# Optimization experiments

Hardware: AMD Instinct MI355X
Metric: run time of the kernel (lower is better)

## Reference

```python
import jax, jax.numpy as jnp
import numpy as np

NW, K, C, H = 4096, 32, 256, 8
HD = C // H
POS_BND = 25            # int(0.8 * patch_size * dilation**0.5) = int(0.8*32)
RPE_NUM = 2 * POS_BND + 1  # 51; table has 3*51 = 153 rows


def setup_inputs() -> dict:
    key = jax.random.key(0)
    ks = jax.random.split(key, 10)
    s = 0.02
    return {
        "data": jax.random.normal(ks[0], (NW * K, C), jnp.float32),
        "mask": jax.random.normal(ks[1], (NW, K, K), jnp.float32),
        "rel_pos": jax.random.randint(ks[2], (NW, K, K, 3), -POS_BND, POS_BND + 1, jnp.int32),
        "qkv_w": jax.random.normal(ks[3], (C, 3 * C), jnp.float32) * s,
        "qkv_b": jnp.zeros((3 * C,), jnp.float32),
        "proj_w": jax.random.normal(ks[4], (C, C), jnp.float32) * s,
        "proj_b": jnp.zeros((C,), jnp.float32),
        "rpe_table": jax.random.normal(ks[5], (3 * RPE_NUM, H), jnp.float32) * s,
        "ln1_g": jnp.ones((C,), jnp.float32),
        "ln1_b": jnp.zeros((C,), jnp.float32),
        "ln2_g": jnp.ones((C,), jnp.float32),
        "ln2_b": jnp.zeros((C,), jnp.float32),
        "fc1_w": jax.random.normal(ks[6], (C, 4 * C), jnp.float32) * s,
        "fc1_b": jnp.zeros((4 * C,), jnp.float32),
        "fc2_w": jax.random.normal(ks[7], (4 * C, C), jnp.float32) * s,
        "fc2_b": jnp.zeros((C,), jnp.float32),
    }


def _ln(x, g, b):
    m = jnp.mean(x, axis=-1, keepdims=True)
    v = jnp.var(x, axis=-1, keepdims=True)
    return (x - m) * jax.lax.rsqrt(v + 1e-5) * g + b


def reference(data, mask, rel_pos, qkv_w, qkv_b, proj_w, proj_b, rpe_table,
              ln1_g, ln1_b, ln2_g, ln2_b, fc1_w, fc1_b, fc2_w, fc2_b):
    scale = float(HD) ** -0.5
    # pre-norm attention branch
    x = _ln(data, ln1_g, ln1_b)
    qkv = (x @ qkv_w + qkv_b).reshape(NW, K, 3, H, HD)
    q, k, v = qkv[:, :, 0], qkv[:, :, 1], qkv[:, :, 2]   # [NW,K,H,HD]
    attn = jnp.einsum('wqhd,wkhd->whqk', q * scale, k)   # [NW,H,K,K]
    # RPE: clamp xyz offsets, offset each axis into its table band, gather+sum
    idx = jnp.clip(rel_pos, -POS_BND, POS_BND) + POS_BND + jnp.arange(3) * RPE_NUM
    bias = rpe_table[idx].sum(axis=3)                    # [NW,K,K,H]
    attn = attn + bias.transpose(0, 3, 1, 2) + mask[:, None]
    attn = jax.nn.softmax(attn, axis=-1)
    out = jnp.einsum('whqk,wkhd->wqhd', attn, v).reshape(NW * K, C)
    data = data + (out @ proj_w + proj_b)
    # pre-norm MLP branch
    h = _ln(data, ln2_g, ln2_b)
    h = jax.nn.gelu(h @ fc1_w + fc1_b) @ fc2_w + fc2_b
    return data + h
```

## Files before the change

kernel.cpp:

```cpp
#include <hip/hip_runtime.h>

#define NWIN 4096
#define KTOK 32
#define CH 256
#define NH 8
#define NTOK (NWIN*KTOK)

typedef unsigned short bf16u;
typedef __attribute__((ext_vector_type(4))) float f32x4;
typedef __attribute__((ext_vector_type(4))) unsigned short u16x4;
typedef __attribute__((ext_vector_type(8))) unsigned short u16x8;
typedef __attribute__((ext_vector_type(8))) __bf16 bf16x8;

__device__ __forceinline__ unsigned short f2bf(float f) {
  unsigned u = __builtin_bit_cast(unsigned, f);
  u += 0x7fffu + ((u >> 16) & 1u);
  return (unsigned short)(u >> 16);
}

__device__ __forceinline__ f32x4 mfma16(bf16x8 a, bf16x8 b, f32x4 c) {
  return __builtin_amdgcn_mfma_f32_16x16x32_bf16(a, b, c, 0, 0, 0);
}

__device__ __forceinline__ void gl16(const void* g, void* l) {
  __builtin_amdgcn_global_load_lds(
      (const __attribute__((address_space(1))) unsigned int*)g,
      (__attribute__((address_space(3))) unsigned int*)l, 16, 0, 0);
}

__device__ __forceinline__ float gelu_f(float x) {
  float u = x + 0.044715f * x * x * x;
  return x * __builtin_amdgcn_rcpf(1.f + __expf(-1.5957691216057308f * u));
}

__global__ __launch_bounds__(256) void wprep_kernel(const float* __restrict__ W,
                                                    bf16u* __restrict__ Wt,
                                                    int Kd, int Nd) {
  int idx = blockIdx.x * 256 + threadIdx.x;
  if (idx >= Kd * Nd) return;
  int k = idx / Nd, n = idx - k * Nd;
  Wt[n * Kd + k] = f2bf(W[idx]);
}

__global__ __launch_bounds__(256) void ln_kernel(const float* __restrict__ x,
                                                 const float* __restrict__ g,
                                                 const float* __restrict__ b,
                                                 bf16u* __restrict__ y) {
  const int row = blockIdx.x * 4 + (threadIdx.x >> 6);
  const int lane = threadIdx.x & 63;
  const size_t base = (size_t)row * CH + lane * 4;
  const f32x4 v = *(const f32x4*)(x + base);
  float s = v[0] + v[1] + v[2] + v[3];
  float q = v[0]*v[0] + v[1]*v[1] + v[2]*v[2] + v[3]*v[3];
  #pragma unroll
  for (int d = 32; d; d >>= 1) { s += __shfl_xor(s, d); q += __shfl_xor(q, d); }
  const float mean = s * (1.f/256.f);
  const float rs = rsqrtf(q * (1.f/256.f) - mean*mean + 1e-5f);
  const f32x4 gv = *(const f32x4*)(g + lane*4);
  const f32x4 bv = *(const f32x4*)(b + lane*4);
  u16x4 o;
  #pragma unroll
  for (int d = 0; d < 4; ++d) o[d] = f2bf((v[d]-mean)*rs*gv[d] + bv[d]);
  *(u16x4*)(y + base) = o;
}

template<int EPI>
__global__ __launch_bounds__(256, 3)
void gemm_kernel(const bf16u* __restrict__ A, const bf16u* __restrict__ Bt,
                 const float* __restrict__ bias, const float* __restrict__ resid,
                 void* __restrict__ out, int M, int N, int K, int nx) {
  __shared__ __align__(16) char lds[49152];
  const int tid = threadIdx.x;
  const int lane = tid & 63;
  const int wv = tid >> 6;
  const int lo = lane & 15, hi = lane >> 4;
  const int nwg = gridDim.x;
  const int cpx = nwg >> 3;
  const int swz = (blockIdx.x & 7) * cpx + (blockIdx.x >> 3);
  const int by = swz / nx, bx = swz - by * nx;
  const int bm = by * 128, bn = bx * 128;
  const int wm = (wv >> 1) * 64, wn = (wv & 1) * 64;

  f32x4 acc[4][4] = {};

  const int srow = tid >> 2;
  const int sk = (tid & 3) * 16;
  const size_t rstep = (size_t)64 * K * 2;
  const char* gA = (const char*)(A + (size_t)(bm + srow) * K) + sk;
  const char* gB = (const char*)(Bt + (size_t)(bn + srow) * K) + sk;

  auto STAGE = [&](int b, int kt) {
    char* As = lds + b * 16384;
    char* Bs = As + 8192;
    const char* ga = gA + kt * 64;
    const char* gb = gB + kt * 64;
    gl16(ga,         As + tid*16);
    gl16(ga + rstep, As + 4096 + tid*16);
    gl16(gb,         Bs + tid*16);
    gl16(gb + rstep, Bs + 4096 + tid*16);
  };

  const int nt = K >> 5;
  STAGE(0, 0);
  STAGE(1, 1);
  int cur = 0;
  for (int t = 0; t < nt; ++t) {
    if (t + 2 < nt) {
      STAGE((cur + 2) % 3, t + 2);
      asm volatile("s_waitcnt vmcnt(8)" ::: "memory");
    } else if (t + 1 < nt) {
      asm volatile("s_waitcnt vmcnt(4)" ::: "memory");
    } else {
      asm volatile("s_waitcnt vmcnt(0)" ::: "memory");
    }
    __builtin_amdgcn_sched_barrier(0);
    __builtin_amdgcn_s_barrier();
    const char* As = lds + cur * 16384;
    const char* Bs = As + 8192;
    bf16x8 af[4], bfv[4];
    #pragma unroll
    for (int i = 0; i < 4; ++i) {
      af[i]  = *(const bf16x8*)(As + (wm + i*16 + lo)*64 + hi*16);
      bfv[i] = *(const bf16x8*)(Bs + (wn + i*16 + lo)*64 + hi*16);
    }
    #pragma unroll
    for (int i = 0; i < 4; ++i)
      #pragma unroll
      for (int j = 0; j < 4; ++j)
        acc[i][j] = mfma16(af[i], bfv[j], acc[i][j]);
    __builtin_amdgcn_s_barrier();
    cur = (cur + 1) % 3;
  }

  __syncthreads();
  float* Ls = (float*)(lds + wv * 4352);
  const int mb = bm + wm, nb = bn + wn;
  const int lrow = lane >> 3;
  const int lcol = (lane & 7) * 8;
  const f32x4 bv0 = *(const f32x4*)(bias + nb + lcol);
  const f32x4 bv1 = *(const f32x4*)(bias + nb + lcol + 4);

  #pragma unroll
  for (int i = 0; i < 4; ++i) {
    #pragma unroll
    for (int j = 0; j < 4; ++j)
      #pragma unroll
      for (int r = 0; r < 4; ++r)
        Ls[(hi*4 + r)*68 + j*16 + lo] = acc[i][j][r];
    #pragma unroll
    for (int p = 0; p < 2; ++p) {
      const int rr = p*8 + lrow;
      const int m = mb + i*16 + rr;
      f32x4 v0 = *(const f32x4*)(Ls + rr*68 + lcol);
      f32x4 v1 = *(const f32x4*)(Ls + rr*68 + lcol + 4);
      v0 += bv0; v1 += bv1;
      if constexpr (EPI == 2) {
        const float* rp = resid + (size_t)m*N + nb + lcol;
        v0 += *(const f32x4*)rp;
        v1 += *(const f32x4*)(rp + 4);
        float* op = (float*)out + (size_t)m*N + nb + lcol;
        *(f32x4*)op = v0;
        *(f32x4*)(op + 4) = v1;
      } else {
        if constexpr (EPI == 1) {
          #pragma unroll
          for (int d = 0; d < 4; ++d) { v0[d] = gelu_f(v0[d]); v1[d] = gelu_f(v1[d]); }
        }
        u16x8 o8;
        #pragma unroll
        for (int d = 0; d < 4; ++d) { o8[d] = f2bf(v0[d]); o8[4+d] = f2bf(v1[d]); }
        *(u16x8*)((bf16u*)out + (size_t)m*N + nb + lcol) = o8;
      }
    }
  }
}

__global__ __launch_bounds__(256, 2)
void gemmP_kernel(const bf16u* __restrict__ A, const bf16u* __restrict__ Bt,
                  const float* __restrict__ bias, const float* __restrict__ resid,
                  float* __restrict__ out, bf16u* __restrict__ xln,
                  const float* __restrict__ g2, const float* __restrict__ b2) {
  __shared__ __align__(16) char lds[73728];
  const int tid = threadIdx.x, lane = tid & 63, wv = tid >> 6;
  const int lo = lane & 15, hi = lane >> 4;
  const int nwg = gridDim.x, cpx = nwg >> 3;
  const int by = (blockIdx.x & 7) * cpx + (blockIdx.x >> 3);
  const int bm = by * 128;
  const int wmh = wv >> 1;
  const int wm = wmh * 64, wn = (wv & 1) * 128;

  f32x4 acc[4][8] = {};

  const int arow = tid >> 2;
  const int sk = (tid & 3) * 16;
  const char* gA = (const char*)(A + (size_t)(bm + arow) * 256) + sk;
  const char* gB = (const char*)(Bt + (size_t)arow * 256) + sk;

  auto STAGE = [&](int b, int kt) {
    char* As = lds + b * 24576;
    char* Bs = As + 8192;
    const char* ga = gA + kt * 64;
    const char* gb = gB + kt * 64;
    gl16(ga,         As + arow*64 + sk);
    gl16(ga + 32768, As + 4096 + arow*64 + sk);
    #pragma unroll
    for (int p = 0; p < 4; ++p)
      gl16(gb + p*32768, Bs + p*4096 + arow*64 + sk);
  };

  STAGE(0, 0);
  STAGE(1, 1);
  int cur = 0;
  for (int t = 0; t < 8; ++t) {
    if (t + 2 < 8) {
      STAGE((cur + 2) % 3, t + 2);
      asm volatile("s_waitcnt vmcnt(12)" ::: "memory");
    } else if (t + 1 < 8) {
      asm volatile("s_waitcnt vmcnt(6)" ::: "memory");
    } else {
      asm volatile("s_waitcnt vmcnt(0)" ::: "memory");
    }
    __builtin_amdgcn_sched_barrier(0);
    __builtin_amdgcn_s_barrier();
    const char* As = lds + cur * 24576;
    const char* Bs = As + 8192;
    bf16x8 af[4], bf8[8];
    #pragma unroll
    for (int i = 0; i < 4; ++i)
      af[i] = *(const bf16x8*)(As + (wm + i*16 + lo)*64 + hi*16);
    #pragma unroll
    for (int j = 0; j < 8; ++j)
      bf8[j] = *(const bf16x8*)(Bs + (wn + j*16 + lo)*64 + hi*16);
    #pragma unroll
    for (int i = 0; i < 4; ++i)
      #pragma unroll
      for (int j = 0; j < 8; ++j)
        acc[i][j] = mfma16(af[i], bf8[j], acc[i][j]);
    __builtin_amdgcn_s_barrier();
    cur = (cur + 1) % 3;
  }

  __syncthreads();
  float* LsE = (float*)lds;
  const int c4 = (tid & 3) * 4;
  const int row64 = tid >> 2;
  const int reg = row64 >> 5, rloc = row64 & 31;
  #pragma unroll
  for (int rr = 0; rr < 2; ++rr) {
    #pragma unroll
    for (int i2 = 0; i2 < 2; ++i2) {
      const int i = rr*2 + i2;
      #pragma unroll
      for (int j = 0; j < 8; ++j)
        #pragma unroll
        for (int r = 0; r < 4; ++r)
          LsE[wmh*8320 + (i2*16 + hi*4 + r)*260 + wn + j*16 + lo] = acc[i][j][r];
    }
    __syncthreads();
    const int grow = bm + reg*64 + rr*32 + rloc;
    f32x4 d2[16];
    float sum = 0.f, sq = 0.f;
    #pragma unroll
    for (int k = 0; k < 16; ++k) {
      const int col = c4 + k*16;
      f32x4 v = *(const f32x4*)&LsE[reg*8320 + rloc*260 + col];
      v += *(const f32x4*)(bias + col);
      v += *(const f32x4*)(resid + (size_t)grow*256 + col);
      d2[k] = v;
      sum += v[0] + v[1] + v[2] + v[3];
      sq  += v[0]*v[0] + v[1]*v[1] + v[2]*v[2] + v[3]*v[3];
      *(f32x4*)(out + (size_t)grow*256 + col) = v;
    }
    sum += __shfl_xor(sum, 1); sq += __shfl_xor(sq, 1);
    sum += __shfl_xor(sum, 2); sq += __shfl_xor(sq, 2);
    const float mean = sum * (1.f/256.f);
    const float rs = rsqrtf(sq * (1.f/256.f) - mean*mean + 1e-5f);
    #pragma unroll
    for (int k = 0; k < 16; ++k) {
      const int col = c4 + k*16;
      const f32x4 gv = *(const f32x4*)(g2 + col);
      const f32x4 bv = *(const f32x4*)(b2 + col);
      u16x4 o;
      #pragma unroll
      for (int d = 0; d < 4; ++d)
        o[d] = f2bf((d2[k][d] - mean) * rs * gv[d] + bv[d]);
      *(u16x4*)(xln + (size_t)grow*256 + col) = o;
    }
    __syncthreads();
  }
}

__global__ __launch_bounds__(256, 2)
void attn_kernel(const bf16u* __restrict__ qkv, const float* __restrict__ mask,
                 const int* __restrict__ relp, const float* __restrict__ rpe,
                 bf16u* __restrict__ outp) {
  const int w = blockIdx.x;
  const int tid = threadIdx.x, lane = tid & 63, wv = tid >> 6;
  const int lo = lane & 15, hi = lane >> 4;

  __shared__ __align__(16) bf16u sQK[32*520];
  __shared__ __align__(16) bf16u sV[32][264];
  __shared__ __align__(16) bf16u sP[4][32][44];
  __shared__ float sTabT[8][156];
  __shared__ int sRel[1024];
  __shared__ float sMask[32][33];

  const size_t qbase = (size_t)w * (32*768);
  {
    #pragma unroll
    for (int t = 0; t < 8; ++t) {
      int i = tid + t*256;
      int tok = i >> 6;
      int cb = (i & 63) * 16;
      *(u16x8*)((char*)sQK + tok*1040 + cb) =
          *(const u16x8*)((const char*)(qkv + qbase) + tok*1536 + cb);
    }
    #pragma unroll
    for (int t = 0; t < 4; ++t) {
      int i = tid + t*256;
      int tok = i >> 5, c8 = i & 31;
      *(u16x8*)&sV[tok][c8*8] = *(const u16x8*)(qkv + qbase + tok*768 + 512 + c8*8);
    }
    for (int i = tid; i < 1224; i += 256)
      sTabT[i & 7][i >> 3] = rpe[i];
    #pragma unroll
    for (int t = 0; t < 4; ++t) {
      int i = tid + t*256;
      const int* rp = relp + ((size_t)w*1024 + i)*3;
      int r0 = rp[0], r1 = rp[1], r2 = rp[2];
      r0 = min(max(r0, -25), 25) + 25;
      r1 = min(max(r1, -25), 25) + 76;
      r2 = min(max(r2, -25), 25) + 127;
      sRel[i] = r0 | (r1 << 8) | (r2 << 16);
    }
    #pragma unroll
    for (int d = 0; d < 4; ++d) {
      int i = tid*4 + d;
      sMask[i >> 5][i & 31] = mask[(size_t)w*1024 + i];
    }
  }
  __syncthreads();

  const float scale = 0.17677669529663687f;
  #pragma unroll
  for (int e = 0; e < 2; ++e) {
    const int h = wv*2 + e;
    bf16x8 qf[2], kf[2];
    #pragma unroll
    for (int rf = 0; rf < 2; ++rf) {
      int tok = rf*16 + lo;
      qf[rf] = *(const bf16x8*)((const char*)sQK + tok*1040 + h*64 + hi*16);
      kf[rf] = *(const bf16x8*)((const char*)sQK + tok*1040 + 512 + h*64 + hi*16);
    }
    f32x4 S[2][2] = {};
    #pragma unroll
    for (int rf = 0; rf < 2; ++rf)
      #pragma unroll
      for (int cf = 0; cf < 2; ++cf)
        S[rf][cf] = mfma16(qf[rf], kf[cf], S[rf][cf]);
    #pragma unroll
    for (int rf = 0; rf < 2; ++rf)
      #pragma unroll
      for (int cf = 0; cf < 2; ++cf)
        #pragma unroll
        for (int r = 0; r < 4; ++r) {
          const int qq = rf*16 + hi*4 + r;
          const int kk = cf*16 + lo;
          const int pk = sRel[qq*32 + kk];
          const float bsum = sTabT[h][pk & 255] + sTabT[h][(pk >> 8) & 255]
                           + sTabT[h][(pk >> 16) & 255];
          S[rf][cf][r] = S[rf][cf][r] * scale + bsum + sMask[qq][kk];
        }
    #pragma unroll
    for (int rf = 0; rf < 2; ++rf)
      #pragma unroll
      for (int r = 0; r < 4; ++r) {
        float m0 = fmaxf(S[rf][0][r], S[rf][1][r]);
        #pragma unroll
        for (int d = 1; d < 16; d <<= 1) m0 = fmaxf(m0, __shfl_xor(m0, d));
        const float p0 = __expf(S[rf][0][r] - m0);
        const float p1 = __expf(S[rf][1][r] - m0);
        float ss = p0 + p1;
        #pragma unroll
        for (int d = 1; d < 16; d <<= 1) ss += __shfl_xor(ss, d);
        const float inv = 1.f / ss;
        S[rf][0][r] = p0 * inv;
        S[rf][1][r] = p1 * inv;
      }
    #pragma unroll
    for (int rf = 0; rf < 2; ++rf)
      #pragma unroll
      for (int cf = 0; cf < 2; ++cf)
        #pragma unroll
        for (int r = 0; r < 4; ++r)
          sP[wv][rf*16 + hi*4 + r][cf*16 + lo] = f2bf(S[rf][cf][r]);
    f32x4 O[2][2] = {};
    #pragma unroll
    for (int rf = 0; rf < 2; ++rf) {
      bf16x8 pf;
      *(u16x4*)&pf       = *(const u16x4*)&sP[wv][rf*16 + lo][hi*8];
      *((u16x4*)&pf + 1) = *(const u16x4*)&sP[wv][rf*16 + lo][hi*8 + 4];
      #pragma unroll
      for (int cf = 0; cf < 2; ++cf) {
        bf16x8 vf;
        #pragma unroll
        for (int j = 0; j < 8; ++j)
          ((bf16u*)&vf)[j] = sV[hi*8 + j][h*32 + cf*16 + lo];
        O[rf][cf] = mfma16(pf, vf, O[rf][cf]);
      }
    }
    #pragma unroll
    for (int rf = 0; rf < 2; ++rf)
      #pragma unroll
      for (int cf = 0; cf < 2; ++cf)
        #pragma unroll
        for (int r = 0; r < 4; ++r) {
          const int qq = rf*16 + hi*4 + r;
          outp[(size_t)(w*32 + qq)*256 + h*32 + cf*16 + lo] = f2bf(O[rf][cf][r]);
        }
  }
}

extern "C" void kernel_launch(void* const* d_in, const int* in_sizes, int n_in,
                              void* d_out, int out_size, void* d_ws, size_t ws_size,
                              hipStream_t stream) {
  const float* data   = (const float*)d_in[0];
  const float* mask   = (const float*)d_in[1];
  const int*   relp   = (const int*)d_in[2];
  const float* qkv_w  = (const float*)d_in[3];
  const float* qkv_b  = (const float*)d_in[4];
  const float* proj_w = (const float*)d_in[5];
  const float* proj_b = (const float*)d_in[6];
  const float* rpe    = (const float*)d_in[7];
  const float* ln1_g  = (const float*)d_in[8];
  const float* ln1_b  = (const float*)d_in[9];
  const float* ln2_g  = (const float*)d_in[10];
  const float* ln2_b  = (const float*)d_in[11];
  const float* fc1_w  = (const float*)d_in[12];
  const float* fc1_b  = (const float*)d_in[13];
  const float* fc2_w  = (const float*)d_in[14];
  const float* fc2_b  = (const float*)d_in[15];

  char* ws = (char*)d_ws;
  bf16u* wt_qkv  = (bf16u*)(ws);
  bf16u* wt_proj = (bf16u*)(ws + 393216);
  bf16u* wt_fc1  = (bf16u*)(ws + 524288);
  bf16u* wt_fc2  = (bf16u*)(ws + 1048576);
  char*  big     = ws + 2097152;
  bf16u* xbuf    = (bf16u*)big;
  bf16u* qkvbuf  = (bf16u*)(big + 67108864);
  bf16u* h1      = (bf16u*)big;
  bf16u* xnorm   = (bf16u*)(big + 268435456);
  float* data2   = (float*)d_out;

  wprep_kernel<<<768, 256, 0, stream>>>(qkv_w, wt_qkv, 256, 768);
  wprep_kernel<<<256, 256, 0, stream>>>(proj_w, wt_proj, 256, 256);
  wprep_kernel<<<1024, 256, 0, stream>>>(fc1_w, wt_fc1, 256, 1024);
  wprep_kernel<<<1024, 256, 0, stream>>>(fc2_w, wt_fc2, 1024, 256);

  ln_kernel<<<32768, 256, 0, stream>>>(data, ln1_g, ln1_b, xnorm);
  gemm_kernel<0><<<6*1024, 256, 0, stream>>>(xnorm, wt_qkv, qkv_b, nullptr,
                                             qkvbuf, NTOK, 768, 256, 6);
  attn_kernel<<<NWIN, 256, 0, stream>>>(qkvbuf, mask, relp, rpe, xbuf);
  gemmP_kernel<<<1024, 256, 0, stream>>>(xbuf, wt_proj, proj_b, data,
                                         data2, xnorm, ln2_g, ln2_b);
  gemm_kernel<1><<<8*1024, 256, 0, stream>>>(xnorm, wt_fc1, fc1_b, nullptr,
                                             h1, NTOK, 1024, 256, 8);
  gemm_kernel<2><<<2*1024, 256, 0, stream>>>(h1, wt_fc2, fc2_b, data2,
                                             d_out, NTOK, 256, 1024, 2);
}
```

Baseline: 632.7 us.

## Add register-resident-A GEMM for K=256 layers and double-buffer generic GEMM

Adds a gemmW kernel for the QKV and FC1 projections (K=256). Each wave holds its full 64x256 A slice in registers, and the whole 64x256 B tile is loaded once into XOR-swizzled LDS, so the k-loop has no per-step barriers or pipelining. The generic GEMM (still used for FC2) drops from triple to double buffering with a 32KB LDS footprint, raising the occupancy bound from 3 to 4 blocks. The epilogue of the new kernel writes scalar bf16 values straight to global memory, which may coalesce poorly. The large A register array may also hurt occupancy.

After: 720.4 us. +13.9%, slower.

```diff
diff --git a/kernel.cpp b/kernel.cpp
--- a/kernel.cpp
+++ b/kernel.cpp
@@ -65,11 +65,78 @@
 }
 
 template<int EPI>
-__global__ __launch_bounds__(256, 3)
+__global__ __launch_bounds__(256, 2)
+void gemmW_kernel(const bf16u* __restrict__ A, const bf16u* __restrict__ Bt,
+                  const float* __restrict__ bias, bf16u* __restrict__ out,
+                  int N, int nx) {
+  __shared__ __align__(16) char lds[32768];
+  const int tid = threadIdx.x, lane = tid & 63, wv = tid >> 6;
+  const int lo = lane & 15, hi = lane >> 4;
+  const int nwg = gridDim.x, cpx = nwg >> 3;
+  const int swz = (blockIdx.x & 7) * cpx + (blockIdx.x >> 3);
+  const int by = swz / nx, bx = swz - by * nx;
+  const int bm = by * 256, bn = bx * 64;
+
+  bf16x8 a[4][8];
+  {
+    const bf16u* ap = A + (size_t)(bm + wv*64 + lo) * 256 + hi*8;
+    #pragma unroll
+    for (int mc = 0; mc < 4; ++mc)
+      #pragma unroll
+      for (int j = 0; j < 8; ++j)
+        a[mc][j] = *(const bf16x8*)(ap + (size_t)mc*16*256 + j*32);
+  }
+  float bv[4];
+  #pragma unroll
+  for (int nf = 0; nf < 4; ++nf) bv[nf] = bias[bn + nf*16 + lo];
+
+  #pragma unroll
+  for (int t = 0; t < 8; ++t) {
+    const int c = t*256 + tid;
+    const int row = c >> 5, g = c & 31;
+    gl16((const char*)Bt + (size_t)(bn + row) * 512 + ((g ^ (row & 7)) * 16),
+         lds + c*16);
+  }
+  __syncthreads();
+
+  f32x4 acc[4][4] = {};
+  #pragma unroll
+  for (int j = 0; j < 8; ++j) {
+    bf16x8 b[4];
+    #pragma unroll
+    for (int nf = 0; nf < 4; ++nf) {
+      const int row = nf*16 + lo;
+      const int g = (j*4 + hi) ^ (row & 7);
+      b[nf] = *(const bf16x8*)(lds + row*512 + g*16);
+    }
+    #pragma unroll
+    for (int mc = 0; mc < 4; ++mc)
+      #pragma unroll
+      for (int nf = 0; nf < 4; ++nf)
+        acc[mc][nf] = mfma16(a[mc][j], b[nf], acc[mc][nf]);
+  }
+
+  #pragma unroll
+  for (int mc = 0; mc < 4; ++mc)
+    #pragma unroll
+    for (int nf = 0; nf < 4; ++nf) {
+      const int n = bn + nf*16 + lo;
+      #pragma unroll
+      for (int r = 0; r < 4; ++r) {
+        const int m = bm + wv*64 + mc*16 + hi*4 + r;
+        float v = acc[mc][nf][r] + bv[nf];
+        if constexpr (EPI == 1) v = gelu_f(v);
+        out[(size_t)m*N + n] = f2bf(v);
+      }
+    }
+}
+
+template<int EPI>
+__global__ __launch_bounds__(256, 4)
 void gemm_kernel(const bf16u* __restrict__ A, const bf16u* __restrict__ Bt,
                  const float* __restrict__ bias, const float* __restrict__ resid,
                  void* __restrict__ out, int M, int N, int K, int nx) {
-  __shared__ __align__(16) char lds[49152];
+  __shared__ __align__(16) char lds[32768];
   const int tid = threadIdx.x;
   const int lane = tid & 63;
   const int wv = tid >> 6;
@@ -89,26 +156,23 @@
   const char* gA = (const char*)(A + (size_t)(bm + srow) * K) + sk;
   const char* gB = (const char*)(Bt + (size_t)(bn + srow) * K) + sk;
 
-  auto STAGE = [&](int b, int kt) {
+  auto STAGE = [&](int b, int k0) {
     char* As = lds + b * 16384;
     char* Bs = As + 8192;
-    const char* ga = gA + kt * 64;
-    const char* gb = gB + kt * 64;
+    const char* ga = gA + k0 * 2;
+    const char* gb = gB + k0 * 2;
     gl16(ga,         As + tid*16);
     gl16(ga + rstep, As + 4096 + tid*16);
     gl16(gb,         Bs + tid*16);
     gl16(gb + rstep, Bs + 4096 + tid*16);
   };
 
-  const int nt = K >> 5;
   STAGE(0, 0);
-  STAGE(1, 1);
   int cur = 0;
-  for (int t = 0; t < nt; ++t) {
-    if (t + 2 < nt) {
-      STAGE((cur + 2) % 3, t + 2);
-      asm volatile("s_waitcnt vmcnt(8)" ::: "memory");
-    } else if (t + 1 < nt) {
+  for (int k0 = 0; ; k0 += 32) {
+    const bool has_next = (k0 + 32 < K);
+    if (has_next) {
+      STAGE(cur ^ 1, k0 + 32);
       asm volatile("s_waitcnt vmcnt(4)" ::: "memory");
     } else {
       asm volatile("s_waitcnt vmcnt(0)" ::: "memory");
@@ -128,8 +192,9 @@
       #pragma unroll
       for (int j = 0; j < 4; ++j)
         acc[i][j] = mfma16(af[i], bfv[j], acc[i][j]);
+    if (!has_next) break;
     __builtin_amdgcn_s_barrier();
-    cur = (cur + 1) % 3;
+    cur ^= 1;
   }
 
   __syncthreads();
@@ -279,11 +344,11 @@
     for (int k = 0; k < 16; ++k) {
       const int col = c4 + k*16;
       const f32x4 gv = *(const f32x4*)(g2 + col);
-      const f32x4 bv = *(const f32x4*)(b2 + col);
+      const f32x4 bvv = *(const f32x4*)(b2 + col);
       u16x4 o;
       #pragma unroll
       for (int d = 0; d < 4; ++d)
-        o[d] = f2bf((d2[k][d] - mean) * rs * gv[d] + bv[d]);
+        o[d] = f2bf((d2[k][d] - mean) * rs * gv[d] + bvv[d]);
       *(u16x4*)(xln + (size_t)grow*256 + col) = o;
     }
     __syncthreads();
@@ -459,13 +524,11 @@
   wprep_kernel<<<1024, 256, 0, stream>>>(fc2_w, wt_fc2, 1024, 256);
 
   ln_kernel<<<32768, 256, 0, stream>>>(data, ln1_g, ln1_b, xnorm);
-  gemm_kernel<0><<<6*1024, 256, 0, stream>>>(xnorm, wt_qkv, qkv_b, nullptr,
-                                             qkvbuf, NTOK, 768, 256, 6);
+  gemmW_kernel<0><<<12*512, 256, 0, stream>>>(xnorm, wt_qkv, qkv_b, qkvbuf, 768, 12);
   attn_kernel<<<NWIN, 256, 0, stream>>>(qkvbuf, mask, relp, rpe, xbuf);
   gemmP_kernel<<<1024, 256, 0, stream>>>(xbuf, wt_proj, proj_b, data,
                                          data2, xnorm, ln2_g, ln2_b);
-  gemm_kernel<1><<<8*1024, 256, 0, stream>>>(xnorm, wt_fc1, fc1_b, nullptr,
-                                             h1, NTOK, 1024, 256, 8);
+  gemmW_kernel<1><<<16*512, 256, 0, stream>>>(xnorm, wt_fc1, fc1_b, h1, 1024, 16);
   gemm_kernel<2><<<2*1024, 256, 0, stream>>>(h1, wt_fc2, fc2_b, data2,
                                              d_out, NTOK, 256, 1024, 2);
 }
```

## Enlarge GEMM tiles to 256x256 with 8 waves per block

Applied to the files above, without the earlier changes.

Replaces the 128x128, 4-wave GEMM with a 256x256 tile run by 512 threads. Each wave now computes a 128x64 sub-tile, which raises MFMA work per LDS fragment load and halves global re-reads of A and B. The triple-buffered LDS doubles to 96KB, and wave priority is raised around the MFMA block. The cost is lower occupancy (launch bounds 512,2), fewer workgroups (only 512 for fc2), and more accumulator registers, which may cause spills.

New measurement: 626.5 us. No clear change (-1.0%).

```diff
diff --git a/kernel.cpp b/kernel.cpp
--- a/kernel.cpp
+++ b/kernel.cpp
@@ -65,39 +65,38 @@
 }
 
 template<int EPI>
-__global__ __launch_bounds__(256, 3)
-void gemm_kernel(const bf16u* __restrict__ A, const bf16u* __restrict__ Bt,
-                 const float* __restrict__ bias, const float* __restrict__ resid,
-                 void* __restrict__ out, int M, int N, int K, int nx) {
-  __shared__ __align__(16) char lds[49152];
+__global__ __launch_bounds__(512, 2)
+void gemm256_kernel(const bf16u* __restrict__ A, const bf16u* __restrict__ Bt,
+                    const float* __restrict__ bias, const float* __restrict__ resid,
+                    void* __restrict__ out, int N, int K, int nx) {
+  __shared__ __align__(16) char lds[98304];
   const int tid = threadIdx.x;
   const int lane = tid & 63;
   const int wv = tid >> 6;
   const int lo = lane & 15, hi = lane >> 4;
+  const int wr = wv >> 2, wc = wv & 3;
   const int nwg = gridDim.x;
   const int cpx = nwg >> 3;
   const int swz = (blockIdx.x & 7) * cpx + (blockIdx.x >> 3);
   const int by = swz / nx, bx = swz - by * nx;
-  const int bm = by * 128, bn = bx * 128;
-  const int wm = (wv >> 1) * 64, wn = (wv & 1) * 64;
-
-  f32x4 acc[4][4] = {};
+  const int bm = by * 256, bn = bx * 256;
+
+  f32x4 acc[8][4] = {};
 
   const int srow = tid >> 2;
-  const int sk = (tid & 3) * 16;
-  const size_t rstep = (size_t)64 * K * 2;
-  const char* gA = (const char*)(A + (size_t)(bm + srow) * K) + sk;
-  const char* gB = (const char*)(Bt + (size_t)(bn + srow) * K) + sk;
+  const int sg = (tid & 3) * 16;
+  const char* pA0 = (const char*)(A + (size_t)(bm + srow) * K) + sg;
+  const char* pA1 = (const char*)(A + (size_t)(bm + 128 + srow) * K) + sg;
+  const char* pB0 = (const char*)(Bt + (size_t)(bn + srow) * K) + sg;
+  const char* pB1 = (const char*)(Bt + (size_t)(bn + 128 + srow) * K) + sg;
 
   auto STAGE = [&](int b, int kt) {
-    char* As = lds + b * 16384;
-    char* Bs = As + 8192;
-    const char* ga = gA + kt * 64;
-    const char* gb = gB + kt * 64;
-    gl16(ga,         As + tid*16);
-    gl16(ga + rstep, As + 4096 + tid*16);
-    gl16(gb,         Bs + tid*16);
-    gl16(gb + rstep, Bs + 4096 + tid*16);
+    char* base = lds + b * 32768;
+    const int ko = kt * 64;
+    gl16(pA0 + ko, base + tid*16);
+    gl16(pA1 + ko, base + 8192 + tid*16);
+    gl16(pB0 + ko, base + 16384 + tid*16);
+    gl16(pB1 + ko, base + 24576 + tid*16);
   };
 
   const int nt = K >> 5;
@@ -115,33 +114,36 @@
     }
     __builtin_amdgcn_sched_barrier(0);
     __builtin_amdgcn_s_barrier();
-    const char* As = lds + cur * 16384;
-    const char* Bs = As + 8192;
-    bf16x8 af[4], bfv[4];
-    #pragma unroll
-    for (int i = 0; i < 4; ++i) {
-      af[i]  = *(const bf16x8*)(As + (wm + i*16 + lo)*64 + hi*16);
-      bfv[i] = *(const bf16x8*)(Bs + (wn + i*16 + lo)*64 + hi*16);
-    }
-    #pragma unroll
-    for (int i = 0; i < 4; ++i)
+    const char* As = lds + cur * 32768;
+    const char* Bs = As + 16384;
+    bf16x8 af[8], bf[4];
+    #pragma unroll
+    for (int i = 0; i < 8; ++i)
+      af[i] = *(const bf16x8*)(As + (wr*128 + i*16 + lo)*64 + hi*16);
+    #pragma unroll
+    for (int j = 0; j < 4; ++j)
+      bf[j] = *(const bf16x8*)(Bs + (wc*64 + j*16 + lo)*64 + hi*16);
+    __builtin_amdgcn_s_setprio(1);
+    #pragma unroll
+    for (int i = 0; i < 8; ++i)
       #pragma unroll
       for (int j = 0; j < 4; ++j)
-        acc[i][j] = mfma16(af[i], bfv[j], acc[i][j]);
+        acc[i][j] = mfma16(af[i], bf[j], acc[i][j]);
+    __builtin_amdgcn_s_setprio(0);
     __builtin_amdgcn_s_barrier();
     cur = (cur + 1) % 3;
   }
 
   __syncthreads();
   float* Ls = (float*)(lds + wv * 4352);
-  const int mb = bm + wm, nb = bn + wn;
+  const int mb = bm + wr*128, nb = bn + wc*64;
   const int lrow = lane >> 3;
   const int lcol = (lane & 7) * 8;
   const f32x4 bv0 = *(const f32x4*)(bias + nb + lcol);
   const f32x4 bv1 = *(const f32x4*)(bias + nb + lcol + 4);
 
   #pragma unroll
-  for (int i = 0; i < 4; ++i) {
+  for (int i = 0; i < 8; ++i) {
     #pragma unroll
     for (int j = 0; j < 4; ++j)
       #pragma unroll
@@ -279,11 +281,11 @@
     for (int k = 0; k < 16; ++k) {
       const int col = c4 + k*16;
       const f32x4 gv = *(const f32x4*)(g2 + col);
-      const f32x4 bv = *(const f32x4*)(b2 + col);
+      const f32x4 bvv = *(const f32x4*)(b2 + col);
       u16x4 o;
       #pragma unroll
       for (int d = 0; d < 4; ++d)
-        o[d] = f2bf((d2[k][d] - mean) * rs * gv[d] + bv[d]);
+        o[d] = f2bf((d2[k][d] - mean) * rs * gv[d] + bvv[d]);
       *(u16x4*)(xln + (size_t)grow*256 + col) = o;
     }
     __syncthreads();
@@ -459,13 +461,13 @@
   wprep_kernel<<<1024, 256, 0, stream>>>(fc2_w, wt_fc2, 1024, 256);
 
   ln_kernel<<<32768, 256, 0, stream>>>(data, ln1_g, ln1_b, xnorm);
-  gemm_kernel<0><<<6*1024, 256, 0, stream>>>(xnorm, wt_qkv, qkv_b, nullptr,
-                                             qkvbuf, NTOK, 768, 256, 6);
+  gemm256_kernel<0><<<512*3, 512, 0, stream>>>(xnorm, wt_qkv, qkv_b, nullptr,
+                                               qkvbuf, 768, 256, 3);
   attn_kernel<<<NWIN, 256, 0, stream>>>(qkvbuf, mask, relp, rpe, xbuf);
   gemmP_kernel<<<1024, 256, 0, stream>>>(xbuf, wt_proj, proj_b, data,
                                          data2, xnorm, ln2_g, ln2_b);
-  gemm_kernel<1><<<8*1024, 256, 0, stream>>>(xnorm, wt_fc1, fc1_b, nullptr,
-                                             h1, NTOK, 1024, 256, 8);
-  gemm_kernel<2><<<2*1024, 256, 0, stream>>>(h1, wt_fc2, fc2_b, data2,
-                                             d_out, NTOK, 256, 1024, 2);
-}
+  gemm256_kernel<1><<<512*4, 512, 0, stream>>>(xnorm, wt_fc1, fc1_b, nullptr,
+                                               h1, 1024, 256, 4);
+  gemm256_kernel<2><<<512*1, 512, 0, stream>>>(h1, wt_fc2, fc2_b, data2,
+                                               d_out, 256, 1024, 1);
+}
```
